# Optimization experiments

Hardware: AMD Instinct MI355X
Metric: run time of the kernel (lower is better)

## Reference

```python
import jax, jax.numpy as jnp
import numpy as np

EPS = 1e-5

def _ln(x, g, b):
    m = x.mean(-1, keepdims=True)
    v = ((x - m) ** 2).mean(-1, keepdims=True)
    return (x - m) * jax.lax.rsqrt(v + EPS) * g + b

def setup_inputs() -> dict:
    V, CTX, D, H, L, HS = 8192, 1024, 1024, 16, 8, 64
    B, T = 4, 1024
    keys = iter(jax.random.split(jax.random.key(0), 16))
    s = lambda *sh: jax.random.normal(next(keys), sh, jnp.float32) * 0.02
    return dict(
        x=jax.random.randint(next(keys), (B, T), 0, CTX, jnp.int32),
        tok_embd=s(V, D), pos_embd=s(CTX, D),
        wq=s(L, H, D, HS), wk=s(L, H, D, HS), wv=s(L, H, D, HS),
        w_o=s(L, H * HS, D), b_o=jnp.zeros((L, D), jnp.float32),
        ln1_g=jnp.ones((L, D), jnp.float32), ln1_b=jnp.zeros((L, D), jnp.float32),
        ln2_g=jnp.ones((L, D), jnp.float32), ln2_b=jnp.zeros((L, D), jnp.float32),
        w1=s(L, D, 4 * D), b1=jnp.zeros((L, 4 * D), jnp.float32),
        w2=s(L, 4 * D, D), b2=jnp.zeros((L, D), jnp.float32),
        lnf_g=jnp.ones((D,), jnp.float32), lnf_b=jnp.zeros((D,), jnp.float32),
        w_lm=s(D, V), b_lm=jnp.zeros((V,), jnp.float32),
    )

def reference(x, tok_embd, pos_embd, wq, wk, wv, w_o, b_o, ln1_g, ln1_b,
              ln2_g, ln2_b, w1, b1, w2, b2, lnf_g, lnf_b, w_lm, b_lm):
    B, T = x.shape
    HS = wq.shape[-1]
    scale = 1.0 / jnp.sqrt(jnp.float32(HS))
    mask = jnp.tril(jnp.ones((T, T), bool))
    # NOTE: source indexes pos_embd with token ids (quirk), reproduced here.
    h = tok_embd[x] + pos_embd[x]

    def block(h, p):
        wq_, wk_, wv_, wo_, bo_, g1, be1, g2, be2, w1_, b1_, w2_, b2_ = p
        hn = _ln(h, g1, be1)
        q = jnp.einsum('btd,hde->bhte', hn, wq_)
        k = jnp.einsum('btd,hde->bhte', hn, wk_)
        v = jnp.einsum('btd,hde->bhte', hn, wv_)
        sc = jnp.einsum('bhqe,bhke->bhqk', q, k) * scale
        sc = jnp.where(mask, sc, -jnp.inf)
        a = jax.nn.softmax(sc, axis=-1)
        o = jnp.einsum('bhqk,bhke->bhqe', a, v)
        o = o.transpose(0, 2, 1, 3).reshape(B, T, -1)  # concat heads
        h = hn + o @ wo_ + bo_
        hn2 = _ln(h, g2, be2)
        h = hn2 + jax.nn.relu(hn2 @ w1_ + b1_) @ w2_ + b2_
        return h, None

    h, _ = jax.lax.scan(block, h, (wq, wk, wv, w_o, b_o, ln1_g, ln1_b,
                                   ln2_g, ln2_b, w1, b1, w2, b2))
    h = _ln(h, lnf_g, lnf_b)
    return h @ w_lm + b_lm
```

## Files before the change

### kernel.cpp

```cpp
#include <hip/hip_runtime.h>
#include <hip/hip_bf16.h>
#include <math.h>

#define BB 4
#define TT 1024
#define DD 1024
#define HH 16
#define HSS 64
#define LL 8
#define VV 8192
#define FFD 4096
#define MM (BB*TT)
#define ASTR 3072

typedef __attribute__((ext_vector_type(8))) _Float16 f16x8;
typedef __attribute__((ext_vector_type(4))) _Float16 f16x4;
typedef __attribute__((ext_vector_type(4))) float floatx4;

__device__ __forceinline__ void gload_lds16(const void* g, void* l) {
  __builtin_amdgcn_global_load_lds(
      (const __attribute__((address_space(1))) void*)(uintptr_t)g,
      (__attribute__((address_space(3))) void*)(uintptr_t)l, 16, 0, 0);
}

__global__ __launch_bounds__(256) void embed_kernel(const int* __restrict__ x,
    const float* __restrict__ tok, const float* __restrict__ pos, _Float16* __restrict__ h)
{
  int i = blockIdx.x * 256 + threadIdx.x;
  int row = i >> 8;
  int c4 = i & 255;
  int id = x[row];
  float4 a = ((const float4*)(tok + (size_t)id * DD))[c4];
  float4 b = ((const float4*)(pos + (size_t)id * DD))[c4];
  f16x4 o;
  o[0] = (_Float16)(a.x + b.x); o[1] = (_Float16)(a.y + b.y);
  o[2] = (_Float16)(a.z + b.z); o[3] = (_Float16)(a.w + b.w);
  *(f16x4*)(h + (size_t)row * DD + c4 * 4) = o;
}

__device__ __forceinline__ void ln_body(const _Float16* __restrict__ in,
    const float* __restrict__ g, const float* __restrict__ bta,
    _Float16* __restrict__ out16, int row, int tid, float* sred)
{
  f16x4 xh = *(const f16x4*)(in + (size_t)row * DD + tid * 4);
  float x0 = (float)xh[0], x1 = (float)xh[1], x2 = (float)xh[2], x3 = (float)xh[3];
  float s = x0 + x1 + x2 + x3;
  #pragma unroll
  for (int o = 32; o; o >>= 1) s += __shfl_down(s, o);
  if ((tid & 63) == 0) sred[tid >> 6] = s;
  __syncthreads();
  float mean = (sred[0] + sred[1] + sred[2] + sred[3]) * (1.f / DD);
  float d0 = x0 - mean, d1 = x1 - mean, d2 = x2 - mean, d3 = x3 - mean;
  float sq = d0 * d0 + d1 * d1 + d2 * d2 + d3 * d3;
  #pragma unroll
  for (int o = 32; o; o >>= 1) sq += __shfl_down(sq, o);
  if ((tid & 63) == 0) sred[4 + (tid >> 6)] = sq;
  __syncthreads();
  float var = (sred[4] + sred[5] + sred[6] + sred[7]) * (1.f / DD);
  float inv = rsqrtf(var + 1e-5f);
  float4 gv = ((const float4*)g)[tid];
  float4 bv = ((const float4*)bta)[tid];
  f16x4 o16;
  o16[0] = (_Float16)(d0 * inv * gv.x + bv.x);
  o16[1] = (_Float16)(d1 * inv * gv.y + bv.y);
  o16[2] = (_Float16)(d2 * inv * gv.z + bv.z);
  o16[3] = (_Float16)(d3 * inv * gv.w + bv.w);
  *(f16x4*)(out16 + (size_t)row * DD + tid * 4) = o16;
}

__device__ __forceinline__ void tcvt_body(const float* __restrict__ in,
    _Float16* __restrict__ out, int K, int N, int bx, int by, int tid, float (*tile)[65])
{
  int bk = bx * 64, bn = by * 64;
  int r = tid >> 4, c4 = (tid & 15) << 2;
  #pragma unroll
  for (int p = 0; p < 4; ++p) {
    float4 v = *(const float4*)(in + (size_t)(bk + p * 16 + r) * N + bn + c4);
    tile[p * 16 + r][c4 + 0] = v.x; tile[p * 16 + r][c4 + 1] = v.y;
    tile[p * 16 + r][c4 + 2] = v.z; tile[p * 16 + r][c4 + 3] = v.w;
  }
  __syncthreads();
  #pragma unroll
  for (int p = 0; p < 4; ++p) {
    int n = p * 16 + r;
    f16x4 o;
    o[0] = (_Float16)tile[c4 + 0][n]; o[1] = (_Float16)tile[c4 + 1][n];
    o[2] = (_Float16)tile[c4 + 2][n]; o[3] = (_Float16)tile[c4 + 3][n];
    *(f16x4*)(out + (size_t)(bn + n) * K + bk + c4) = o;
  }
}

__global__ __launch_bounds__(256) void tcvt(const float* __restrict__ in,
    _Float16* __restrict__ out, int K, int N)
{
  __shared__ float tile[64][65];
  tcvt_body(in, out, K, N, blockIdx.x, blockIdx.y, threadIdx.x, tile);
}

__global__ __launch_bounds__(256) void ln_kernel(const _Float16* __restrict__ in,
    const float* __restrict__ g, const float* __restrict__ bta, _Float16* __restrict__ out16)
{
  __shared__ float sred[8];
  ln_body(in, g, bta, out16, blockIdx.x, threadIdx.x, sred);
}

__global__ __launch_bounds__(256) void layer_prep(const _Float16* __restrict__ h,
    const float* __restrict__ g1, const float* __restrict__ b1v, _Float16* __restrict__ hn16,
    const float* __restrict__ wq, const float* __restrict__ wk, const float* __restrict__ wv,
    _Float16* __restrict__ wqkv_t,
    const float* __restrict__ wo, _Float16* __restrict__ wo_t,
    const float* __restrict__ w1, _Float16* __restrict__ w1_t,
    const float* __restrict__ w2, _Float16* __restrict__ w2_t)
{
  __shared__ float tile[64][65];
  __shared__ float sred[8];
  const int bid = blockIdx.x;
  const int tid = threadIdx.x;
  if (bid < 4096) {
    ln_body(h, g1, b1v, hn16, bid, tid, sred);
  } else if (bid < 4864) {
    const int b2 = bid - 4096;
    const int m  = b2 >> 8;
    const int rem = b2 & 255;
    const int hh = rem >> 4, dt = rem & 15;
    const float* src = ((m == 0) ? wq : (m == 1) ? wk : wv)
                     + (size_t)hh * DD * HSS + (size_t)(dt * 64) * HSS;
    const float scale = (m == 0) ? 0.125f : 1.0f;
    const int r = tid >> 2, cq = (tid & 3) << 4;
    #pragma unroll
    for (int p = 0; p < 4; ++p) {
      float4 v = *(const float4*)(src + (size_t)r * HSS + cq + p * 4);
      tile[r][cq + p * 4 + 0] = v.x * scale; tile[r][cq + p * 4 + 1] = v.y * scale;
      tile[r][cq + p * 4 + 2] = v.z * scale; tile[r][cq + p * 4 + 3] = v.w * scale;
    }
    __syncthreads();
    const int e = tid >> 2, dq = (tid & 3) << 4;
    _Float16* dst = wqkv_t + ((size_t)(m * 1024 + hh * 64 + e)) * DD + dt * 64 + dq;
    f16x8 o0, o1;
    #pragma unroll
    for (int j = 0; j < 8; ++j) o0[j] = (_Float16)tile[dq + j][e];
    #pragma unroll
    for (int j = 0; j < 8; ++j) o1[j] = (_Float16)tile[dq + 8 + j][e];
    *(f16x8*)dst = o0;
    *(f16x8*)(dst + 8) = o1;
  } else if (bid < 5120) {
    int b2i = bid - 4864;
    tcvt_body(wo, wo_t, DD, DD, b2i & 15, b2i >> 4, tid, tile);
  } else if (bid < 6144) {
    int b2i = bid - 5120;
    tcvt_body(w1, w1_t, DD, FFD, b2i & 15, b2i >> 4, tid, tile);
  } else {
    int b2i = bid - 6144;
    tcvt_body(w2, w2_t, FFD, DD, b2i & 63, b2i >> 6, tid, tile);
  }
}

#define GBM 128
#define GBK 64
template<int BN, int SWZ, bool OUT16, bool RELU, bool BIAS, bool RES>
__global__ __launch_bounds__(256) void mfma_gemm(
    const _Float16* __restrict__ A, const _Float16* __restrict__ Bt,
    const float* __restrict__ bias, const _Float16* __restrict__ res,
    void* __restrict__ Cout, int M, int N, int K)
{
  constexpr int NI = BN / 32;
  __shared__ __align__(16) _Float16 Asl[2][GBM * GBK];
  __shared__ __align__(16) _Float16 Bsl[2][BN * GBK];
  const int tid = threadIdx.x;
  const int w = tid >> 6, l = tid & 63;
  const int gx = gridDim.x, gy = gridDim.y;
  const int ihw = blockIdx.y * gx + blockIdx.x;
  const int xcd = ihw & 7, local_i = ihw >> 3;
  int bm_t, bn_t;
  if (SWZ == 0) {
    const int cpx = (gx * gy) >> 3;
    const int si = xcd * cpx + local_i;
    bm_t = si / gx; bn_t = si % gx;
  } else {
    bm_t = local_i % gy;
    bn_t = xcd * (gx >> 3) + local_i / gy;
  }
  const int bm = bm_t * GBM, bn = bn_t * BN;
  const int wr = (w >> 1) * 64, wc = (w & 1) * (NI * 16);
  const int srow = l >> 3;
  const int scol = l & 7;

  floatx4 acc[4][NI];
  #pragma unroll
  for (int mi = 0; mi < 4; ++mi)
    #pragma unroll
    for (int ni = 0; ni < NI; ++ni) acc[mi][ni] = (floatx4){0.f, 0.f, 0.f, 0.f};

  auto stage = [&](int buf, int kt) {
    const int k0 = kt * GBK;
    #pragma unroll
    for (int i = 0; i < 4; ++i) {
      int rA = w * 32 + i * 8 + srow;
      const void* gpA = (const char*)(A + (size_t)(bm + rA) * K + k0) + ((scol ^ srow) << 4);
      gload_lds16(gpA, (void*)&Asl[buf][(size_t)(w * 32 + i * 8) * GBK]);
    }
    #pragma unroll
    for (int i = 0; i < BN / 32; ++i) {
      int rB = w * (BN / 4) + i * 8 + srow;
      const void* gpB = (const char*)(Bt + (size_t)(bn + rB) * K + k0) + ((scol ^ srow) << 4);
      gload_lds16(gpB, (void*)&Bsl[buf][(size_t)(w * (BN / 4) + i * 8) * GBK]);
    }
  };

  stage(0, 0);
  const int NT = K / GBK;
  for (int t = 0; t < NT; ++t) {
    const int cur = t & 1;
    if (t + 1 < NT) {
      stage(cur ^ 1, t + 1);
      if constexpr (BN == 64) asm volatile("s_waitcnt vmcnt(6)" ::: "memory");
      else                    asm volatile("s_waitcnt vmcnt(8)" ::: "memory");
    } else {
      asm volatile("s_waitcnt vmcnt(0)" ::: "memory");
    }
    __builtin_amdgcn_s_barrier();
    asm volatile("" ::: "memory");

    const char* ab = (const char*)&Asl[cur][0];
    const char* bb = (const char*)&Bsl[cur][0];
    #pragma unroll
    for (int kk = 0; kk < 2; ++kk) {
      const int kbyte = kk * 64 + (l >> 4) * 16;
      f16x8 af[4], bf[NI];
      #pragma unroll
      for (int mi = 0; mi < 4; ++mi) {
        int row = wr + mi * 16 + (l & 15);
        af[mi] = *(const f16x8*)(ab + row * 128 + (kbyte ^ ((row & 7) << 4)));
      }
      #pragma unroll
      for (int ni = 0; ni < NI; ++ni) {
        int row = wc + ni * 16 + (l & 15);
        bf[ni] = *(const f16x8*)(bb + row * 128 + (kbyte ^ ((row & 7) << 4)));
      }
      #pragma unroll
      for (int mi = 0; mi < 4; ++mi)
        #pragma unroll
        for (int ni = 0; ni < NI; ++ni)
          acc[mi][ni] = __builtin_amdgcn_mfma_f32_16x16x32_f16(af[mi], bf[ni], acc[mi][ni], 0, 0, 0);
    }
    __builtin_amdgcn_s_barrier();
    asm volatile("" ::: "memory");
  }

  #pragma unroll
  for (int ni = 0; ni < NI; ++ni) {
    const int col = bn + wc + ni * 16 + (l & 15);
    const float bv = BIAS ? bias[col] : 0.f;
    #pragma unroll
    for (int mi = 0; mi < 4; ++mi) {
      #pragma unroll
      for (int r = 0; r < 4; ++r) {
        const int row = bm + wr + mi * 16 + (l >> 4) * 4 + r;
        float v = acc[mi][ni][r] + bv;
        if (RELU) v = fmaxf(v, 0.f);
        if (RES) v += (float)res[(size_t)row * N + col];
        if (OUT16) ((_Float16*)Cout)[(size_t)row * N + col] = (_Float16)v;
        else       ((float*)Cout)[(size_t)row * N + col] = v;
      }
    }
  }
}

#define PBM 256
#define PBN 256
#define PBK 64
template<int SWZ, int VOUT, bool OUT16, bool RELU, bool BIAS, bool RES>
__global__ __launch_bounds__(512) void mfma_gemm256(
    const _Float16* __restrict__ A, const _Float16* __restrict__ Bt,
    const float* __restrict__ bias, const _Float16* __restrict__ res,
    void* __restrict__ Cout, _Float16* __restrict__ vt, int M, int N, int K)
{
  __shared__ __align__(16) _Float16 Asl[2][PBM * PBK];
  __shared__ __align__(16) _Float16 Bsl[2][PBN * PBK];
  const int tid = threadIdx.x;
  const int w = tid >> 6, l = tid & 63;
  const int wm = w >> 2, wn = w & 3;
  const int l16 = l & 15, g16 = l >> 4;
  const int rgrp = l >> 3, chunk = l & 7;
  const int gx = gridDim.x, gy = gridDim.y;
  const int ihw = blockIdx.y * gx + blockIdx.x;
  int bm_t, bn_t;
  if (SWZ == 0) {
    const int cpx = (gx * gy) >> 3;
    const int si = (ihw & 7) * cpx + (ihw >> 3);
    bm_t = si / gx; bn_t = si % gx;
  } else {
    bn_t = ihw / gy; bm_t = ihw % gy;
  }
  const int bm = bm_t * PBM, bn = bn_t * PBN;

  floatx4 acc[8][4];
  #pragma unroll
  for (int mi = 0; mi < 8; ++mi)
    #pragma unroll
    for (int ni = 0; ni < 4; ++ni) acc[mi][ni] = (floatx4){0.f, 0.f, 0.f, 0.f};

  auto stage_half = [&](int buf, int kt, int hp) {
    const int k0 = kt * PBK;
    const int half = hp & 1;
    #pragma unroll
    for (int i = 0; i < 2; ++i) {
      const int r = half * 128 + i * 64 + w * 8 + rgrp;
      if (hp < 2) {
        const char* g = (const char*)(A + (size_t)(bm + r) * K + k0) + ((chunk ^ rgrp) << 4);
        gload_lds16(g, (void*)&Asl[buf][(size_t)(half * 128 + i * 64 + w * 8) * PBK]);
      } else {
        const char* g = (const char*)(Bt + (size_t)(bn + r) * K + k0) + ((chunk ^ rgrp) << 4);
        gload_lds16(g, (void*)&Bsl[buf][(size_t)(half * 128 + i * 64 + w * 8) * PBK]);
      }
    }
  };

  stage_half(0, 0, 0); stage_half(0, 0, 1); stage_half(0, 0, 2); stage_half(0, 0, 3);

  const int NT = K >> 6;
  for (int t = 0; t < NT; ++t) {
    const int cur = t & 1;
    if (t + 1 < NT) {
      stage_half(cur ^ 1, t + 1, 0);
      asm volatile("s_waitcnt vmcnt(2)" ::: "memory");
    } else {
      asm volatile("s_waitcnt vmcnt(0)" ::: "memory");
    }
    __builtin_amdgcn_s_barrier();
    asm volatile("" ::: "memory");
    __builtin_amdgcn_sched_barrier(0);

    const char* ab = (const char*)&Asl[cur][0];
    const char* bb = (const char*)&Bsl[cur][0];

    f16x8 bf[4][2];
    #pragma unroll
    for (int c = 0; c < 2; ++c) {
      const int kbyte = c * 64 + g16 * 16;
      #pragma unroll
      for (int ni = 0; ni < 4; ++ni) {
        int row = wn * 64 + ni * 16 + l16;
        bf[ni][c] = *(const f16x8*)(bb + row * 128 + (kbyte ^ ((row & 7) << 4)));
      }
    }
    {
      f16x8 af[4][2];
      #pragma unroll
      for (int c = 0; c < 2; ++c) {
        const int kbyte = c * 64 + g16 * 16;
        #pragma unroll
        for (int mi = 0; mi < 4; ++mi) {
          int row = wm * 128 + mi * 16 + l16;
          af[mi][c] = *(const f16x8*)(ab + row * 128 + (kbyte ^ ((row & 7) << 4)));
        }
      }
      if (t + 1 < NT) stage_half(cur ^ 1, t + 1, 1);
      __builtin_amdgcn_s_setprio(1);
      #pragma unroll
      for (int c = 0; c < 2; ++c)
        #pragma unroll
        for (int mi = 0; mi < 4; ++mi)
          #pragma unroll
          for (int ni = 0; ni < 4; ++ni)
            acc[mi][ni] = __builtin_amdgcn_mfma_f32_16x16x32_f16(af[mi][c], bf[ni][c], acc[mi][ni], 0, 0, 0);
      __builtin_amdgcn_s_setprio(0);
    }
    {
      f16x8 af[4][2];
      #pragma unroll
      for (int c = 0; c < 2; ++c) {
        const int kbyte = c * 64 + g16 * 16;
        #pragma unroll
        for (int mi = 0; mi < 4; ++mi) {
          int row = wm * 128 + 64 + mi * 16 + l16;
          af[mi][c] = *(const f16x8*)(ab + row * 128 + (kbyte ^ ((row & 7) << 4)));
        }
      }
      if (t + 1 < NT) { stage_half(cur ^ 1, t + 1, 2); stage_half(cur ^ 1, t + 1, 3); }
      __builtin_amdgcn_s_setprio(1);
      #pragma unroll
      for (int c = 0; c < 2; ++c)
        #pragma unroll
        for (int mi = 0; mi < 4; ++mi)
          #pragma unroll
          for (int ni = 0; ni < 4; ++ni)
            acc[4 + mi][ni] = __builtin_amdgcn_mfma_f32_16x16x32_f16(af[mi][c], bf[ni][c], acc[4 + mi][ni], 0, 0, 0);
      __builtin_amdgcn_s_setprio(0);
    }
    asm volatile("" ::: "memory");
    __builtin_amdgcn_sched_barrier(0);
    __builtin_amdgcn_s_barrier();
  }

  if (VOUT && bn >= 2048) {
    const int bq = bm >> 10;
    #pragma unroll
    for (int ni = 0; ni < 4; ++ni) {
      const int ch = bn - 2048 + wn * 64 + ni * 16 + l16;
      _Float16* vcol = vt + ((size_t)(bq * 1024 + ch)) * TT;
      #pragma unroll
      for (int mi = 0; mi < 8; ++mi) {
        const int trow = (bm & 1023) + wm * 128 + mi * 16 + g16 * 4;
        f16x4 o;
        o[0] = (_Float16)acc[mi][ni][0]; o[1] = (_Float16)acc[mi][ni][1];
        o[2] = (_Float16)acc[mi][ni][2]; o[3] = (_Float16)acc[mi][ni][3];
        *(f16x4*)(vcol + trow) = o;
      }
    }
  } else {
    #pragma unroll
    for (int ni = 0; ni < 4; ++ni) {
      const int col = bn + wn * 64 + ni * 16 + l16;
      const float bv = BIAS ? bias[col] : 0.f;
      #pragma unroll
      for (int mi = 0; mi < 8; ++mi) {
        #pragma unroll
        for (int r = 0; r < 4; ++r) {
          const int row = bm + wm * 128 + mi * 16 + g16 * 4 + r;
          float v = acc[mi][ni][r] + bv;
          if (RELU) v = fmaxf(v, 0.f);
          if (RES) v += (float)res[(size_t)row * N + col];
          if (OUT16) ((_Float16*)Cout)[(size_t)row * N + col] = (_Float16)v;
          else       ((float*)Cout)[(size_t)row * N + col] = v;
        }
      }
    }
  }
}

#define AQB 128
#define AKB 64
__global__ __launch_bounds__(512) void attn_mfma(const _Float16* __restrict__ qkv16,
    const _Float16* __restrict__ vt16, _Float16* __restrict__ op)
{
  __shared__ __align__(16) _Float16 Kb[2][AKB * HSS];
  __shared__ __align__(16) _Float16 Vtb[2][AKB * HSS];
  __shared__ __align__(16) _Float16 Ps[8][16 * AKB];
  const int ib = blockIdx.x;
  int bh, qt;
  if (ib < 256) { bh = ib >> 2; qt = 7 - (ib & 3); }
  else          { int j = ib - 256; bh = j >> 2; qt = j & 3; }
  const int b  = bh >> 4;
  const int hh = bh & 15;
  const int q0 = qt * AQB;
  const int t  = threadIdx.x;
  const int w  = t >> 6, l = t & 63;
  const int l16 = l & 15, g16 = l >> 4;
  const size_t rowbase = (size_t)b * TT;
  const int hoff = hh * HSS;
  const size_t vbase = (size_t)bh * 64;
  const int rgrp = l >> 3, chunk = l & 7;

  f16x8 aq[2];
  {
    const _Float16* qrow = qkv16 + (rowbase + q0 + w * 16 + l16) * ASTR + hoff;
    aq[0] = *(const f16x8*)(qrow + g16 * 8);
    aq[1] = *(const f16x8*)(qrow + 32 + g16 * 8);
  }

  floatx4 oacc[4];
  #pragma unroll
  for (int ni = 0; ni < 4; ++ni) oacc[ni] = (floatx4){0.f, 0.f, 0.f, 0.f};
  float mrow[4], srow[4];
  #pragma unroll
  for (int r = 0; r < 4; ++r) { mrow[r] = -3.0e38f; srow[r] = 0.f; }

  auto stage = [&](int buf, int tt) {
    const int j0 = tt * AKB;
    const int rk = w * 8 + rgrp;
    const char* gK = (const char*)(qkv16 + (rowbase + j0 + rk) * ASTR + 1024 + hoff)
                   + ((chunk ^ (rk & 7)) << 4);
    gload_lds16(gK, (void*)((char*)&Kb[buf][0] + (w * 8) * 128));
    const char* gV = (const char*)(vt16 + (vbase + rk) * TT + j0)
                   + ((chunk ^ (rk & 7)) << 4);
    gload_lds16(gV, (void*)((char*)&Vtb[buf][0] + (w * 8) * 128));
  };

  const int ntiles = 2 * qt + 2;
  stage(0, 0);
  for (int tt = 0; tt < ntiles; ++tt) {
    const int cur = tt & 1;
    if (tt + 1 < ntiles) {
      stage(cur ^ 1, tt + 1);
      asm volatile("s_waitcnt vmcnt(2)" ::: "memory");
    } else {
      asm volatile("s_waitcnt vmcnt(0)" ::: "memory");
    }
    __builtin_amdgcn_s_barrier();
    asm volatile("" ::: "memory");

    const char* kb = (const char*)&Kb[cur][0];
    const char* vb = (const char*)&Vtb[cur][0];
    const int j0 = tt * AKB;
    const int dj = j0 - q0;
    if (dj <= w * 16 + 15) {
      floatx4 sacc[4];
      #pragma unroll
      for (int ni = 0; ni < 4; ++ni) sacc[ni] = (floatx4){0.f, 0.f, 0.f, 0.f};
      #pragma unroll
      for (int c = 0; c < 2; ++c) {
        const int kbyte = c * 64 + g16 * 16;
        #pragma unroll
        for (int ni = 0; ni < 4; ++ni) {
          int row = ni * 16 + l16;
          f16x8 bf = *(const f16x8*)(kb + row * 128 + (kbyte ^ ((row & 7) << 4)));
          sacc[ni] = __builtin_amdgcn_mfma_f32_16x16x32_f16(aq[c], bf, sacc[ni], 0, 0, 0);
        }
      }
      if (tt >= 2 * qt) {
        #pragma unroll
        for (int ni = 0; ni < 4; ++ni)
          #pragma unroll
          for (int r = 0; r < 4; ++r)
            if (dj + ni * 16 + l16 > w * 16 + g16 * 4 + r) sacc[ni][r] = -3.0e38f;
      }
      #pragma unroll
      for (int r = 0; r < 4; ++r) {
        float mx = fmaxf(fmaxf(sacc[0][r], sacc[1][r]), fmaxf(sacc[2][r], sacc[3][r]));
        mx = fmaxf(mx, __shfl_xor(mx, 1));
        mx = fmaxf(mx, __shfl_xor(mx, 2));
        mx = fmaxf(mx, __shfl_xor(mx, 4));
        mx = fmaxf(mx, __shfl_xor(mx, 8));
        float mnew = fmaxf(mrow[r], mx);
        float f = __expf(mrow[r] - mnew);
        mrow[r] = mnew;
        srow[r] *= f;
        #pragma unroll
        for (int ni = 0; ni < 4; ++ni) oacc[ni][r] *= f;
      }
      #pragma unroll
      for (int ni = 0; ni < 4; ++ni)
        #pragma unroll
        for (int r = 0; r < 4; ++r)
          sacc[ni][r] = __expf(sacc[ni][r] - mrow[r]);
      #pragma unroll
      for (int r = 0; r < 4; ++r) {
        float ss = sacc[0][r] + sacc[1][r] + sacc[2][r] + sacc[3][r];
        ss += __shfl_xor(ss, 1); ss += __shfl_xor(ss, 2);
        ss += __shfl_xor(ss, 4); ss += __shfl_xor(ss, 8);
        srow[r] += ss;
      }
      char* psb = (char*)&Ps[w][0];
      #pragma unroll
      for (int ni = 0; ni < 4; ++ni)
        #pragma unroll
        for (int r = 0; r < 4; ++r) {
          int q = g16 * 4 + r;
          *(_Float16*)(psb + ((q * 128 + (ni * 16 + l16) * 2) ^ ((q & 7) << 4))) = (_Float16)sacc[ni][r];
        }
      #pragma unroll
      for (int c = 0; c < 2; ++c) {
        const int kbyte = c * 64 + g16 * 16;
        f16x8 ap = *(const f16x8*)(psb + l16 * 128 + (kbyte ^ ((l16 & 7) << 4)));
        #pragma unroll
        for (int ni = 0; ni < 4; ++ni) {
          int erow = ni * 16 + l16;
          f16x8 bv = *(const f16x8*)(vb + erow * 128 + (kbyte ^ ((erow & 7) << 4)));
          oacc[ni] = __builtin_amdgcn_mfma_f32_16x16x32_f16(ap, bv, oacc[ni], 0, 0, 0);
        }
      }
    }
    __builtin_amdgcn_s_barrier();
    asm volatile("" ::: "memory");
  }
  #pragma unroll
  for (int r = 0; r < 4; ++r) {
    float inv = 1.f / srow[r];
    _Float16* od = op + (rowbase + q0 + w * 16 + g16 * 4 + r) * (size_t)DD + hoff;
    #pragma unroll
    for (int ni = 0; ni < 4; ++ni)
      od[ni * 16 + l16] = (_Float16)(oacc[ni][r] * inv);
  }
}

extern "C" void kernel_launch(void* const* d_in, const int* in_sizes, int n_in,
                              void* d_out, int out_size, void* d_ws, size_t ws_size,
                              hipStream_t stream)
{
  const int*   x     = (const int*)d_in[0];
  const float* tok   = (const float*)d_in[1];
  const float* pos   = (const float*)d_in[2];
  const float* wq    = (const float*)d_in[3];
  const float* wk    = (const float*)d_in[4];
  const float* wv    = (const float*)d_in[5];
  const float* w_o   = (const float*)d_in[6];
  const float* b_o   = (const float*)d_in[7];
  const float* ln1_g = (const float*)d_in[8];
  const float* ln1_b = (const float*)d_in[9];
  const float* ln2_g = (const float*)d_in[10];
  const float* ln2_b = (const float*)d_in[11];
  const float* w1    = (const float*)d_in[12];
  const float* b1    = (const float*)d_in[13];
  const float* w2    = (const float*)d_in[14];
  const float* b2    = (const float*)d_in[15];
  const float* lnf_g = (const float*)d_in[16];
  const float* lnf_b = (const float*)d_in[17];
  const float* w_lm  = (const float*)d_in[18];
  const float* b_lm  = (const float*)d_in[19];
  float* out = (float*)d_out;
  char* p = (char*)d_ws;

  const size_t MB = 1024 * 1024;
  _Float16* h16    = (_Float16*)(p);
  _Float16* hn16   = (_Float16*)(p + 16 * MB);
  _Float16* qkv16  = (_Float16*)(p + 24 * MB);
  _Float16* vt16   = (_Float16*)(p + 48 * MB);
  _Float16* ob16   = (_Float16*)(p + 56 * MB);
  _Float16* mlp16  = (_Float16*)(p + 24 * MB);
  _Float16* wqkv_t = (_Float16*)(p + 64 * MB);
  _Float16* wo_t   = (_Float16*)(p + 70 * MB);
  _Float16* w1_t   = (_Float16*)(p + 72 * MB);
  _Float16* w2_t   = (_Float16*)(p + 80 * MB);
  _Float16* wlm_t  = (_Float16*)(p + 88 * MB);

  tcvt<<<dim3(16, 128), 256, 0, stream>>>(w_lm, wlm_t, DD, VV);
  embed_kernel<<<dim3(MM * DD / 4 / 256), 256, 0, stream>>>(x, tok, pos, h16);

  for (int l = 0; l < LL; ++l) {
    const size_t wqo = (size_t)l * HH * DD * HSS;
    layer_prep<<<dim3(7168), 256, 0, stream>>>(
        h16, ln1_g + (size_t)l * DD, ln1_b + (size_t)l * DD, hn16,
        wq + wqo, wk + wqo, wv + wqo, wqkv_t,
        w_o + wqo, wo_t,
        w1 + (size_t)l * DD * FFD, w1_t,
        w2 + (size_t)l * FFD * DD, w2_t);
    mfma_gemm256<0,1,true,false,false,false><<<dim3(ASTR / PBN, MM / PBM), 512, 0, stream>>>(
        hn16, wqkv_t, nullptr, nullptr, qkv16, vt16, MM, ASTR, DD);
    attn_mfma<<<dim3(BB * HH * (TT / AQB)), 512, 0, stream>>>(qkv16, vt16, ob16);
    mfma_gemm<64,0,true,false,true,true><<<dim3(DD / 64, MM / GBM), 256, 0, stream>>>(
        ob16, wo_t, b_o + (size_t)l * DD, hn16, h16, MM, DD, DD);
    ln_kernel<<<MM, 256, 0, stream>>>(h16, ln2_g + (size_t)l * DD, ln2_b + (size_t)l * DD, hn16);
    mfma_gemm256<2,0,true,true,true,false><<<dim3(FFD / PBN, MM / PBM), 512, 0, stream>>>(
        hn16, w1_t, b1 + (size_t)l * FFD, nullptr, mlp16, nullptr, MM, FFD, DD);
    mfma_gemm<64,0,true,false,true,true><<<dim3(DD / 64, MM / GBM), 256, 0, stream>>>(
        mlp16, w2_t, b2 + (size_t)l * DD, hn16, h16, MM, DD, FFD);
  }
  ln_kernel<<<MM, 256, 0, stream>>>(h16, lnf_g, lnf_b, hn16);
  mfma_gemm256<2,0,false,false,true,false><<<dim3(VV / PBN, MM / PBM), 512, 0, stream>>>(
      hn16, wlm_t, b_lm, nullptr, out, nullptr, MM, VV, DD);
}
```

Before: 1.557 ms.

## Double attention K/V tile size to 128 keys, halving barrier rounds

Attention now stages 128 keys per tile instead of 64, processing each tile as two 64-key halves with the same online softmax. This halves the number of stage/wait/barrier iterations per query block and issues more loads per pipeline stage. In exchange it doubles K/V shared memory, which may reduce occupancy, and the V swizzle now uses a 256-byte row stride.

```diff
diff --git a/kernel.cpp b/kernel.cpp
--- a/kernel.cpp
+++ b/kernel.cpp
@@ -430,13 +430,13 @@
 }
 
 #define AQB 128
-#define AKB 64
+#define AKB 128
 __global__ __launch_bounds__(512) void attn_mfma(const _Float16* __restrict__ qkv16,
     const _Float16* __restrict__ vt16, _Float16* __restrict__ op)
 {
   __shared__ __align__(16) _Float16 Kb[2][AKB * HSS];
-  __shared__ __align__(16) _Float16 Vtb[2][AKB * HSS];
-  __shared__ __align__(16) _Float16 Ps[8][16 * AKB];
+  __shared__ __align__(16) _Float16 Vtb[2][HSS * AKB];
+  __shared__ __align__(16) _Float16 Ps[8][16 * 64];
   const int ib = blockIdx.x;
   int bh, qt;
   if (ib < 256) { bh = ib >> 2; qt = 7 - (ib & 3); }
@@ -451,6 +451,7 @@
   const int hoff = hh * HSS;
   const size_t vbase = (size_t)bh * 64;
   const int rgrp = l >> 3, chunk = l & 7;
+  const int vrow4 = l >> 4, vchunk = l & 15;
 
   f16x8 aq[2];
   {
@@ -468,22 +469,29 @@
 
   auto stage = [&](int buf, int tt) {
     const int j0 = tt * AKB;
-    const int rk = w * 8 + rgrp;
-    const char* gK = (const char*)(qkv16 + (rowbase + j0 + rk) * ASTR + 1024 + hoff)
-                   + ((chunk ^ (rk & 7)) << 4);
-    gload_lds16(gK, (void*)((char*)&Kb[buf][0] + (w * 8) * 128));
-    const char* gV = (const char*)(vt16 + (vbase + rk) * TT + j0)
-                   + ((chunk ^ (rk & 7)) << 4);
-    gload_lds16(gV, (void*)((char*)&Vtb[buf][0] + (w * 8) * 128));
+    #pragma unroll
+    for (int i = 0; i < 2; ++i) {
+      const int rk = w * 16 + i * 8 + rgrp;
+      const char* gK = (const char*)(qkv16 + (rowbase + j0 + rk) * ASTR + 1024 + hoff)
+                     + ((chunk ^ (rk & 7)) << 4);
+      gload_lds16(gK, (void*)((char*)&Kb[buf][0] + (w * 16 + i * 8) * 128));
+    }
+    #pragma unroll
+    for (int i = 0; i < 2; ++i) {
+      const int rv = w * 8 + i * 4 + vrow4;
+      const char* gV = (const char*)(vt16 + (vbase + rv) * TT + j0)
+                     + ((vchunk ^ (rv & 7)) << 4);
+      gload_lds16(gV, (void*)((char*)&Vtb[buf][0] + (w * 8 + i * 4) * 256));
+    }
   };
 
-  const int ntiles = 2 * qt + 2;
+  const int ntiles = qt + 1;
   stage(0, 0);
   for (int tt = 0; tt < ntiles; ++tt) {
     const int cur = tt & 1;
     if (tt + 1 < ntiles) {
       stage(cur ^ 1, tt + 1);
-      asm volatile("s_waitcnt vmcnt(2)" ::: "memory");
+      asm volatile("s_waitcnt vmcnt(4)" ::: "memory");
     } else {
       asm volatile("s_waitcnt vmcnt(0)" ::: "memory");
     }
@@ -492,72 +500,76 @@
 
     const char* kb = (const char*)&Kb[cur][0];
     const char* vb = (const char*)&Vtb[cur][0];
-    const int j0 = tt * AKB;
-    const int dj = j0 - q0;
-    if (dj <= w * 16 + 15) {
-      floatx4 sacc[4];
-      #pragma unroll
-      for (int ni = 0; ni < 4; ++ni) sacc[ni] = (floatx4){0.f, 0.f, 0.f, 0.f};
-      #pragma unroll
-      for (int c = 0; c < 2; ++c) {
-        const int kbyte = c * 64 + g16 * 16;
-        #pragma unroll
-        for (int ni = 0; ni < 4; ++ni) {
-          int row = ni * 16 + l16;
-          f16x8 bf = *(const f16x8*)(kb + row * 128 + (kbyte ^ ((row & 7) << 4)));
-          sacc[ni] = __builtin_amdgcn_mfma_f32_16x16x32_f16(aq[c], bf, sacc[ni], 0, 0, 0);
-        }
-      }
-      if (tt >= 2 * qt) {
+    #pragma unroll
+    for (int half = 0; half < 2; ++half) {
+      const int j0h = tt * AKB + half * 64;
+      const int dj = j0h - q0;
+      if (dj <= w * 16 + 15) {
+        floatx4 sacc[4];
+        #pragma unroll
+        for (int ni = 0; ni < 4; ++ni) sacc[ni] = (floatx4){0.f, 0.f, 0.f, 0.f};
+        #pragma unroll
+        for (int c = 0; c < 2; ++c) {
+          const int kbyte = c * 64 + g16 * 16;
+          #pragma unroll
+          for (int ni = 0; ni < 4; ++ni) {
+            int row = half * 64 + ni * 16 + l16;
+            f16x8 bf = *(const f16x8*)(kb + row * 128 + (kbyte ^ ((row & 7) << 4)));
+            sacc[ni] = __builtin_amdgcn_mfma_f32_16x16x32_f16(aq[c], bf, sacc[ni], 0, 0, 0);
+          }
+        }
+        if (dj >= 0) {
+          #pragma unroll
+          for (int ni = 0; ni < 4; ++ni)
+            #pragma unroll
+            for (int r = 0; r < 4; ++r)
+              if (dj + ni * 16 + l16 > w * 16 + g16 * 4 + r) sacc[ni][r] = -3.0e38f;
+        }
+        #pragma unroll
+        for (int r = 0; r < 4; ++r) {
+          float mx = fmaxf(fmaxf(sacc[0][r], sacc[1][r]), fmaxf(sacc[2][r], sacc[3][r]));
+          mx = fmaxf(mx, __shfl_xor(mx, 1));
+          mx = fmaxf(mx, __shfl_xor(mx, 2));
+          mx = fmaxf(mx, __shfl_xor(mx, 4));
+          mx = fmaxf(mx, __shfl_xor(mx, 8));
+          float mnew = fmaxf(mrow[r], mx);
+          float f = __expf(mrow[r] - mnew);
+          mrow[r] = mnew;
+          srow[r] *= f;
+          #pragma unroll
+          for (int ni = 0; ni < 4; ++ni) oacc[ni][r] *= f;
+        }
         #pragma unroll
         for (int ni = 0; ni < 4; ++ni)
           #pragma unroll
           for (int r = 0; r < 4; ++r)
-            if (dj + ni * 16 + l16 > w * 16 + g16 * 4 + r) sacc[ni][r] = -3.0e38f;
-      }
-      #pragma unroll
-      for (int r = 0; r < 4; ++r) {
-        float mx = fmaxf(fmaxf(sacc[0][r], sacc[1][r]), fmaxf(sacc[2][r], sacc[3][r]));
-        mx = fmaxf(mx, __shfl_xor(mx, 1));
-        mx = fmaxf(mx, __shfl_xor(mx, 2));
-        mx = fmaxf(mx, __shfl_xor(mx, 4));
-        mx = fmaxf(mx, __shfl_xor(mx, 8));
-        float mnew = fmaxf(mrow[r], mx);
-        float f = __expf(mrow[r] - mnew);
-        mrow[r] = mnew;
-        srow[r] *= f;
-        #pragma unroll
-        for (int ni = 0; ni < 4; ++ni) oacc[ni][r] *= f;
-      }
-      #pragma unroll
-      for (int ni = 0; ni < 4; ++ni)
-        #pragma unroll
-        for (int r = 0; r < 4; ++r)
-          sacc[ni][r] = __expf(sacc[ni][r] - mrow[r]);
-      #pragma unroll
-      for (int r = 0; r < 4; ++r) {
-        float ss = sacc[0][r] + sacc[1][r] + sacc[2][r] + sacc[3][r];
-        ss += __shfl_xor(ss, 1); ss += __shfl_xor(ss, 2);
-        ss += __shfl_xor(ss, 4); ss += __shfl_xor(ss, 8);
-        srow[r] += ss;
-      }
-      char* psb = (char*)&Ps[w][0];
-      #pragma unroll
-      for (int ni = 0; ni < 4; ++ni)
+            sacc[ni][r] = __expf(sacc[ni][r] - mrow[r]);
         #pragma unroll
         for (int r = 0; r < 4; ++r) {
-          int q = g16 * 4 + r;
-          *(_Float16*)(psb + ((q * 128 + (ni * 16 + l16) * 2) ^ ((q & 7) << 4))) = (_Float16)sacc[ni][r];
-        }
-      #pragma unroll
-      for (int c = 0; c < 2; ++c) {
-        const int kbyte = c * 64 + g16 * 16;
-        f16x8 ap = *(const f16x8*)(psb + l16 * 128 + (kbyte ^ ((l16 & 7) << 4)));
-        #pragma unroll
-        for (int ni = 0; ni < 4; ++ni) {
-          int erow = ni * 16 + l16;
-          f16x8 bv = *(const f16x8*)(vb + erow * 128 + (kbyte ^ ((erow & 7) << 4)));
-          oacc[ni] = __builtin_amdgcn_mfma_f32_16x16x32_f16(ap, bv, oacc[ni], 0, 0, 0);
+          float ss = sacc[0][r] + sacc[1][r] + sacc[2][r] + sacc[3][r];
+          ss += __shfl_xor(ss, 1); ss += __shfl_xor(ss, 2);
+          ss += __shfl_xor(ss, 4); ss += __shfl_xor(ss, 8);
+          srow[r] += ss;
+        }
+        char* psb = (char*)&Ps[w][0];
+        #pragma unroll
+        for (int ni = 0; ni < 4; ++ni)
+          #pragma unroll
+          for (int r = 0; r < 4; ++r) {
+            int q = g16 * 4 + r;
+            *(_Float16*)(psb + ((q * 128 + (ni * 16 + l16) * 2) ^ ((q & 7) << 4))) = (_Float16)sacc[ni][r];
+          }
+        #pragma unroll
+        for (int c = 0; c < 2; ++c) {
+          const int kbyteP = c * 64 + g16 * 16;
+          f16x8 ap = *(const f16x8*)(psb + l16 * 128 + (kbyteP ^ ((l16 & 7) << 4)));
+          const int vbyte = half * 128 + c * 64 + g16 * 16;
+          #pragma unroll
+          for (int ni = 0; ni < 4; ++ni) {
+            int erow = ni * 16 + l16;
+            f16x8 bv = *(const f16x8*)(vb + erow * 256 + (vbyte ^ ((erow & 7) << 4)));
+            oacc[ni] = __builtin_amdgcn_mfma_f32_16x16x32_f16(ap, bv, oacc[ni], 0, 0, 0);
+          }
         }
       }
     }
```

New measurement: 1.571 ms. About the same (+0.9%).
